# Optimization experiments

Hardware: AMD Instinct MI355X
Metric: run time of the kernel (lower is better)

Reference implementation:

```python
import jax, jax.numpy as jnp
import numpy as np

EPS = 1e-5

def _ln(x):
    # LayerNorm over last dim, no affine (elementwise_affine=False), biased variance
    mu = jnp.mean(x, axis=-1, keepdims=True)
    var = jnp.mean(jnp.square(x - mu), axis=-1, keepdims=True)
    return (x - mu) / jnp.sqrt(var + EPS)

def setup_inputs() -> dict:
    key = jax.random.key(0)
    B, I, H = 32768, 512, 512
    ks = jax.random.split(key, 12)
    std = 1.0 / np.sqrt(H)
    u = lambda k, shape: jax.random.uniform(k, shape, jnp.float32, -std, std)
    return {
        "x": jax.random.normal(ks[0], (B, I), jnp.float32),
        "h": jax.random.normal(ks[1], (B, H), jnp.float32),
        "W_i2h": u(ks[2], (I, 2 * H)),
        "b_i2h": u(ks[3], (2 * H,)),
        "W_h2h": u(ks[4], (H, 2 * H)),
        "b_h2h": u(ks[5], (2 * H,)),
        "W_hatW": u(ks[6], (I, H)),
        "b_hatW": u(ks[7], (H,)),
        "W_hatU": u(ks[8], (H, H)),
        "b_hatU": u(ks[9], (H,)),
    }

def reference(x, h, W_i2h, b_i2h, W_h2h, b_h2h, W_hatW, b_hatW, W_hatU, b_hatU):
    H = W_hatU.shape[0]
    i2h = _ln(x @ W_i2h + b_i2h)          # [B, 2H]
    h2h = _ln(h @ W_h2h + b_h2h)          # [B, 2H]
    gates = jax.nn.sigmoid(i2h + h2h)
    z_t = gates[:, :H]
    r_t = gates[:, -H:]
    h_hat_first = _ln(x @ W_hatW + b_hatW)  # [B, H]
    h_hat_last = _ln(h @ W_hatU + b_hatU)   # [B, H]
    h_hat = jnp.tanh(h_hat_first + r_t * h_hat_last)
    h_t = (1.0 - z_t) * h + z_t * h_hat
    return h_t
```

## Files before the change

kernel.cpp:

```cpp
#include <hip/hip_runtime.h>
#include <stdint.h>

typedef unsigned short u16;
typedef __attribute__((ext_vector_type(8))) short short8;
typedef __attribute__((ext_vector_type(4))) short short4v;
typedef __attribute__((ext_vector_type(4))) float f4;
typedef __attribute__((ext_vector_type(4))) float f32x4;

static __device__ __forceinline__ u16 f2b(float f) {
  union { float f; uint32_t u; } c; c.f = f;
  return (u16)((c.u + 0x7FFFu + ((c.u >> 16) & 1u)) >> 16);
}
static __device__ __forceinline__ float b2f(u16 s) {
  union { uint32_t u; float f; } c; c.u = ((uint32_t)s) << 16; return c.f;
}

__global__ __launch_bounds__(256) void cvt_kernel(const float* __restrict__ x,
                                                  const float* __restrict__ h,
                                                  u16* __restrict__ Ab) {
  const size_t half = (size_t)32768 * 512;
  size_t tid = (size_t)blockIdx.x * blockDim.x + threadIdx.x;
  size_t nth = (size_t)gridDim.x * blockDim.x;
  size_t total8 = (half * 2) >> 3;
  for (size_t t = tid; t < total8; t += nth) {
    size_t e = t << 3;
    const float* src = (e < half) ? (x + e) : (h + (e - half));
    f4 v0 = *(const f4*)src;
    f4 v1 = *(const f4*)(src + 4);
    short8 o;
    o[0] = (short)f2b(v0[0]); o[1] = (short)f2b(v0[1]);
    o[2] = (short)f2b(v0[2]); o[3] = (short)f2b(v0[3]);
    o[4] = (short)f2b(v1[0]); o[5] = (short)f2b(v1[1]);
    o[6] = (short)f2b(v1[2]); o[7] = (short)f2b(v1[3]);
    *(short8*)(Ab + e) = o;
  }
}

__global__ __launch_bounds__(256) void transpose_cat(const float* __restrict__ srcA,
                                                     const float* __restrict__ srcB,
                                                     u16* __restrict__ dst,
                                                     int NA, int NB) {
  __shared__ float t[32][33];
  int n0 = blockIdx.x * 32, k0 = blockIdx.y * 32;
  int tx = threadIdx.x, ty = threadIdx.y;
  const float* src; int strideN, nb;
  if (n0 < NA) { src = srcA; strideN = NA; nb = n0; }
  else         { src = srcB; strideN = NB; nb = n0 - NA; }
#pragma unroll
  for (int i = 0; i < 4; ++i) {
    int k = k0 + ty + i * 8;
    t[tx][ty + i * 8] = src[(size_t)k * strideN + nb + tx];
  }
  __syncthreads();
#pragma unroll
  for (int i = 0; i < 4; ++i) {
    int n = ty + i * 8;
    dst[(size_t)(n0 + n) * 512 + k0 + tx] = f2b(t[n][tx]);
  }
}

#define AS1 __attribute__((address_space(1)))
#define AS3 __attribute__((address_space(3)))
#define SBAR0 __builtin_amdgcn_sched_barrier(0)

__global__ __launch_bounds__(512, 2) void gemm_kernel(
    const u16* __restrict__ Ab, const u16* __restrict__ WxT,
    const u16* __restrict__ WhT, u16* __restrict__ Cb,
    int rowStartX, int rowStartH, int tilesPerHalf) {
  __shared__ u16 lds[65536];

  int tid = threadIdx.x, lane = tid & 63, wv = tid >> 6;
  int wm = wv >> 2, wn = wv & 3;
  int l15 = lane & 15, l4 = lane >> 4;

  int nwg = gridDim.x, bid = blockIdx.x;
  int swz = (nwg & 7) ? bid : ((bid & 7) * (nwg >> 3) + (bid >> 3));
  int mb = swz / 6, nb = swz - mb * 6;
  size_t m0; const u16* Wt;
  if (mb < tilesPerHalf) { m0 = (size_t)rowStartX + (size_t)mb * 256; Wt = WxT; }
  else { m0 = (size_t)rowStartH + (size_t)(mb - tilesPerHalf) * 256; Wt = WhT; }
  int crow0 = mb * 256, n0 = nb * 256;

  int rr = wv * 8 + (lane >> 3);
  int g8 = ((lane & 7) ^ (lane >> 3)) * 8;
  const u16* pA[4]; const u16* pB[4];
#pragma unroll
  for (int i = 0; i < 4; ++i) {
    pA[i] = Ab + (m0 + i * 64 + rr) * 512 + g8;
    pB[i] = Wt + (size_t)(n0 + i * 64 + rr) * 512 + g8;
  }
  int dst = wv * 512;

#define STG(t) do { \
    int _bb = ((t) & 1) << 15; \
    int _ko = (t) << 6; \
    _Pragma("unroll") \
    for (int i = 0; i < 4; ++i) { \
      __builtin_amdgcn_global_load_lds((const AS1 void*)(pA[i] + _ko), \
          (AS3 void*)(lds + _bb + i * 4096 + dst), 16, 0, 0); \
      __builtin_amdgcn_global_load_lds((const AS1 void*)(pB[i] + _ko), \
          (AS3 void*)(lds + _bb + 16384 + i * 4096 + dst), 16, 0, 0); \
    } \
  } while (0)

  int sl0 = (l4 ^ (l15 & 7)) * 8;
  int sl1 = ((4 + l4) ^ (l15 & 7)) * 8;
  int aRow = (wm * 128 + l15) * 64;
  int bRow = 16384 + (wn * 64 + l15) * 64;

  f32x4 acc[8][4] = {};

  STG(0); STG(1);
  asm volatile("s_waitcnt vmcnt(8)" ::: "memory");
  SBAR0; __builtin_amdgcn_s_barrier(); SBAR0;

  for (int t = 0; t < 8; ++t) {
    const u16* buf = lds + ((t & 1) << 15);
    short8 afr[4], bfr[4];
    if (t >= 1 && t < 7) STG(t + 1);
#pragma unroll
    for (int nr = 0; nr < 4; ++nr) bfr[nr] = *(const short8*)(buf + bRow + nr * 1024 + sl0);
#pragma unroll
    for (int mr = 0; mr < 4; ++mr) afr[mr] = *(const short8*)(buf + aRow + mr * 1024 + sl0);
    SBAR0; __builtin_amdgcn_s_barrier(); SBAR0;
    __builtin_amdgcn_s_setprio(1);
#pragma unroll
    for (int mr = 0; mr < 4; ++mr)
#pragma unroll
      for (int nr = 0; nr < 4; ++nr)
        acc[mr][nr] = __builtin_amdgcn_mfma_f32_16x16x32_bf16(bfr[nr], afr[mr], acc[mr][nr], 0, 0, 0);
    __builtin_amdgcn_s_setprio(0);
#pragma unroll
    for (int mr = 0; mr < 4; ++mr) afr[mr] = *(const short8*)(buf + aRow + (mr + 4) * 1024 + sl0);
    SBAR0; __builtin_amdgcn_s_barrier(); SBAR0;
    __builtin_amdgcn_s_setprio(1);
#pragma unroll
    for (int mr = 0; mr < 4; ++mr)
#pragma unroll
      for (int nr = 0; nr < 4; ++nr)
        acc[mr + 4][nr] = __builtin_amdgcn_mfma_f32_16x16x32_bf16(bfr[nr], afr[mr], acc[mr + 4][nr], 0, 0, 0);
    __builtin_amdgcn_s_setprio(0);
#pragma unroll
    for (int nr = 0; nr < 4; ++nr) bfr[nr] = *(const short8*)(buf + bRow + nr * 1024 + sl1);
#pragma unroll
    for (int mr = 0; mr < 4; ++mr) afr[mr] = *(const short8*)(buf + aRow + mr * 1024 + sl1);
    SBAR0; __builtin_amdgcn_s_barrier(); SBAR0;
    __builtin_amdgcn_s_setprio(1);
#pragma unroll
    for (int mr = 0; mr < 4; ++mr)
#pragma unroll
      for (int nr = 0; nr < 4; ++nr)
        acc[mr][nr] = __builtin_amdgcn_mfma_f32_16x16x32_bf16(bfr[nr], afr[mr], acc[mr][nr], 0, 0, 0);
    __builtin_amdgcn_s_setprio(0);
#pragma unroll
    for (int mr = 0; mr < 4; ++mr) afr[mr] = *(const short8*)(buf + aRow + (mr + 4) * 1024 + sl1);
    SBAR0; __builtin_amdgcn_s_barrier(); SBAR0;
    __builtin_amdgcn_s_setprio(1);
#pragma unroll
    for (int mr = 0; mr < 4; ++mr)
#pragma unroll
      for (int nr = 0; nr < 4; ++nr)
        acc[mr + 4][nr] = __builtin_amdgcn_mfma_f32_16x16x32_bf16(bfr[nr], afr[mr], acc[mr + 4][nr], 0, 0, 0);
    __builtin_amdgcn_s_setprio(0);
    SBAR0;
    if (t < 7) {
      asm volatile("s_waitcnt vmcnt(0)" ::: "memory");
      __builtin_amdgcn_s_barrier();
    }
    SBAR0;
  }
#undef STG

#pragma unroll
  for (int mr = 0; mr < 8; ++mr) {
    int m = crow0 + wm * 128 + mr * 16 + l15;
#pragma unroll
    for (int nr = 0; nr < 4; ++nr) {
      int n = n0 + wn * 64 + nr * 16 + l4 * 4;
      short4v o;
      o[0] = (short)f2b(acc[mr][nr][0]);
      o[1] = (short)f2b(acc[mr][nr][1]);
      o[2] = (short)f2b(acc[mr][nr][2]);
      o[3] = (short)f2b(acc[mr][nr][3]);
      *(short4v*)(Cb + (size_t)m * 1536 + n) = o;
    }
  }
}

__global__ __launch_bounds__(256) void epi_kernel(
    const u16* __restrict__ Cb, const float* __restrict__ h,
    const float* __restrict__ b_i2h, const float* __restrict__ b_h2h,
    const float* __restrict__ b_hatW, const float* __restrict__ b_hatU,
    float* __restrict__ out, int mBase, int BC) {
  int wv = threadIdx.x >> 6;
  int lane = threadIdx.x & 63;
  int mLocal = blockIdx.x * 4 + wv;
  size_t mGlob = (size_t)mBase + mLocal;
  const u16* Ar = Cb + (size_t)mLocal * 1536;
  const u16* Br = Cb + ((size_t)BC + mLocal) * 1536;
  int j0 = lane * 8;

  float a[3][8], b[3][8];
#pragma unroll
  for (int c = 0; c < 3; ++c) {
    short8 va = *(const short8*)(Ar + c * 512 + j0);
    short8 vb = *(const short8*)(Br + c * 512 + j0);
    const float* biasA = (c == 0) ? (b_i2h + j0) : (c == 1) ? (b_i2h + 512 + j0) : (b_hatW + j0);
    const float* biasB = (c == 0) ? (b_h2h + j0) : (c == 1) ? (b_h2h + 512 + j0) : (b_hatU + j0);
    f4 ba0 = *(const f4*)biasA, ba1 = *(const f4*)(biasA + 4);
    f4 bb0 = *(const f4*)biasB, bb1 = *(const f4*)(biasB + 4);
#pragma unroll
    for (int j = 0; j < 4; ++j) {
      a[c][j]     = b2f((u16)va[j])     + ba0[j];
      a[c][j + 4] = b2f((u16)va[j + 4]) + ba1[j];
      b[c][j]     = b2f((u16)vb[j])     + bb0[j];
      b[c][j + 4] = b2f((u16)vb[j + 4]) + bb1[j];
    }
  }

  float s1a = 0, q1a = 0, s2a = 0, q2a = 0, s1b = 0, q1b = 0, s2b = 0, q2b = 0;
#pragma unroll
  for (int j = 0; j < 8; ++j) {
    s1a += a[0][j] + a[1][j]; q1a += a[0][j] * a[0][j] + a[1][j] * a[1][j];
    s2a += a[2][j];           q2a += a[2][j] * a[2][j];
    s1b += b[0][j] + b[1][j]; q1b += b[0][j] * b[0][j] + b[1][j] * b[1][j];
    s2b += b[2][j];           q2b += b[2][j] * b[2][j];
  }
#pragma unroll
  for (int off = 32; off > 0; off >>= 1) {
    s1a += __shfl_xor(s1a, off); q1a += __shfl_xor(q1a, off);
    s2a += __shfl_xor(s2a, off); q2a += __shfl_xor(q2a, off);
    s1b += __shfl_xor(s1b, off); q1b += __shfl_xor(q1b, off);
    s2b += __shfl_xor(s2b, off); q2b += __shfl_xor(q2b, off);
  }
  const float inv1 = 1.0f / 1024.0f, inv2 = 1.0f / 512.0f, eps = 1e-5f;
  float mu1a = s1a * inv1, mu2a = s2a * inv2, mu1b = s1b * inv1, mu2b = s2b * inv2;
  float rs1a = rsqrtf(q1a * inv1 - mu1a * mu1a + eps);
  float rs2a = rsqrtf(q2a * inv2 - mu2a * mu2a + eps);
  float rs1b = rsqrtf(q1b * inv1 - mu1b * mu1b + eps);
  float rs2b = rsqrtf(q2b * inv2 - mu2b * mu2b + eps);

  const float* hrow = h + mGlob * 512 + j0;
  f4 h0 = *(const f4*)hrow, h1 = *(const f4*)(hrow + 4);
  f4 o0, o1;
#pragma unroll
  for (int j = 0; j < 8; ++j) {
    float zs  = (a[0][j] - mu1a) * rs1a + (b[0][j] - mu1b) * rs1b;
    float rsg = (a[1][j] - mu1a) * rs1a + (b[1][j] - mu1b) * rs1b;
    float z = 1.0f / (1.0f + __expf(-zs));
    float r = 1.0f / (1.0f + __expf(-rsg));
    float hh = tanhf((a[2][j] - mu2a) * rs2a + r * ((b[2][j] - mu2b) * rs2b));
    float hv = (j < 4) ? h0[j] : h1[j - 4];
    float o = hv + z * (hh - hv);
    if (j < 4) o0[j] = o; else o1[j - 4] = o;
  }
  *(f4*)(out + mGlob * 512 + j0) = o0;
  *(f4*)(out + mGlob * 512 + j0 + 4) = o1;
}

extern "C" void kernel_launch(void* const* d_in, const int* in_sizes, int n_in,
                              void* d_out, int out_size, void* d_ws, size_t ws_size,
                              hipStream_t stream) {
  const float* x      = (const float*)d_in[0];
  const float* h      = (const float*)d_in[1];
  const float* W_i2h  = (const float*)d_in[2];
  const float* b_i2h  = (const float*)d_in[3];
  const float* W_h2h  = (const float*)d_in[4];
  const float* b_h2h  = (const float*)d_in[5];
  const float* W_hatW = (const float*)d_in[6];
  const float* b_hatW = (const float*)d_in[7];
  const float* W_hatU = (const float*)d_in[8];
  const float* b_hatU = (const float*)d_in[9];
  float* out = (float*)d_out;

  u16* WxT = (u16*)d_ws;
  u16* WhT = WxT + (size_t)1536 * 512;
  u16* Ab  = WhT + (size_t)1536 * 512;
  u16* Cb  = Ab + (size_t)65536 * 512;

  size_t fixedElems = (size_t)2 * 1536 * 512 + (size_t)65536 * 512;
  int chunks = 1;
  for (;;) {
    size_t need = (fixedElems + (size_t)2 * (32768 / chunks) * 1536) * sizeof(u16);
    if (need <= ws_size || chunks >= 128) break;
    chunks <<= 1;
  }
  int BC = 32768 / chunks;
  int tph = BC / 256;
  int nwg = 2 * tph * 6;

  cvt_kernel<<<2048, 256, 0, stream>>>(x, h, Ab);
  transpose_cat<<<dim3(48, 16), dim3(32, 8), 0, stream>>>(W_i2h, W_hatW, WxT, 1024, 512);
  transpose_cat<<<dim3(48, 16), dim3(32, 8), 0, stream>>>(W_h2h, W_hatU, WhT, 1024, 512);
  for (int cc = 0; cc < chunks; ++cc) {
    gemm_kernel<<<nwg, 512, 0, stream>>>(Ab, WxT, WhT, Cb,
                                         cc * BC, 32768 + cc * BC, tph);
    epi_kernel<<<BC / 4, 256, 0, stream>>>(Cb, h, b_i2h, b_h2h, b_hatW, b_hatU,
                                           out, cc * BC, BC);
  }
}
```

Before: 246.5 us.

## Make GEMM persistent with 256x128 tiles and triple-buffered LDS pipeline

```diff
diff --git a/kernel.cpp b/kernel.cpp
--- a/kernel.cpp
+++ b/kernel.cpp
@@ -63,65 +63,77 @@
 #define AS3 __attribute__((address_space(3)))
 #define SBAR0 __builtin_amdgcn_sched_barrier(0)
 
-__global__ __launch_bounds__(512, 2) void gemm_kernel(
+__global__ __launch_bounds__(512, 1) void gemm_kernel(
     const u16* __restrict__ Ab, const u16* __restrict__ WxT,
     const u16* __restrict__ WhT, u16* __restrict__ Cb,
-    int rowStartX, int rowStartH, int tilesPerHalf) {
-  __shared__ u16 lds[65536];
+    int rowStartX, int rowStartH, int tphm, int KOT) {
+  __shared__ u16 lds[3 * 24576];
 
   int tid = threadIdx.x, lane = tid & 63, wv = tid >> 6;
-  int wm = wv >> 2, wn = wv & 3;
+  int wm = wv >> 1, wn = wv & 1;
   int l15 = lane & 15, l4 = lane >> 4;
 
   int nwg = gridDim.x, bid = blockIdx.x;
   int swz = (nwg & 7) ? bid : ((bid & 7) * (nwg >> 3) + (bid >> 3));
-  int mb = swz / 6, nb = swz - mb * 6;
-  size_t m0; const u16* Wt;
-  if (mb < tilesPerHalf) { m0 = (size_t)rowStartX + (size_t)mb * 256; Wt = WxT; }
-  else { m0 = (size_t)rowStartH + (size_t)(mb - tilesPerHalf) * 256; Wt = WhT; }
-  int crow0 = mb * 256, n0 = nb * 256;
-
-  int rr = wv * 8 + (lane >> 3);
-  int g8 = ((lane & 7) ^ (lane >> 3)) * 8;
-  const u16* pA[4]; const u16* pB[4];
-#pragma unroll
-  for (int i = 0; i < 4; ++i) {
-    pA[i] = Ab + (m0 + i * 64 + rr) * 512 + g8;
-    pB[i] = Wt + (size_t)(n0 + i * 64 + rr) * 512 + g8;
-  }
-  int dst = wv * 512;
-
-#define STG(t) do { \
-    int _bb = ((t) & 1) << 15; \
-    int _ko = (t) << 6; \
-    _Pragma("unroll") \
-    for (int i = 0; i < 4; ++i) { \
-      __builtin_amdgcn_global_load_lds((const AS1 void*)(pA[i] + _ko), \
-          (AS3 void*)(lds + _bb + i * 4096 + dst), 16, 0, 0); \
-      __builtin_amdgcn_global_load_lds((const AS1 void*)(pB[i] + _ko), \
-          (AS3 void*)(lds + _bb + 16384 + i * 4096 + dst), 16, 0, 0); \
-    } \
+
+  int stRow = tid >> 3;
+  int g8 = ((tid & 7) ^ (stRow & 7)) * 8;
+  int dOff = tid * 8;
+
+  const u16 *pA0, *pA1, *pA2, *pA3, *pB0, *pB1;
+#define SETSTAGE(o) do { \
+    int _ot = swz * KOT + (o); \
+    int _mb = _ot / 12, _nb = _ot - _mb * 12; \
+    size_t _am0 = (_mb < tphm) ? (size_t)rowStartX + (size_t)_mb * 256 \
+                               : (size_t)rowStartH + (size_t)(_mb - tphm) * 256; \
+    const u16* _Wt = (_mb < tphm) ? WxT : WhT; \
+    pA0 = Ab + (_am0 +   0 + stRow) * 512 + g8; \
+    pA1 = Ab + (_am0 +  64 + stRow) * 512 + g8; \
+    pA2 = Ab + (_am0 + 128 + stRow) * 512 + g8; \
+    pA3 = Ab + (_am0 + 192 + stRow) * 512 + g8; \
+    pB0 = _Wt + ((size_t)_nb * 128 +  0 + stRow) * 512 + g8; \
+    pB1 = _Wt + ((size_t)_nb * 128 + 64 + stRow) * 512 + g8; \
+  } while (0)
+
+#define STG(kt, bufq) do { \
+    u16* _b = lds + (bufq) * 24576; \
+    int _ko = (kt) << 6; \
+    __builtin_amdgcn_global_load_lds((const AS1 void*)(pA0 + _ko), (AS3 void*)(_b +  0    + dOff), 16, 0, 0); \
+    __builtin_amdgcn_global_load_lds((const AS1 void*)(pA1 + _ko), (AS3 void*)(_b + 4096  + dOff), 16, 0, 0); \
+    __builtin_amdgcn_global_load_lds((const AS1 void*)(pA2 + _ko), (AS3 void*)(_b + 8192  + dOff), 16, 0, 0); \
+    __builtin_amdgcn_global_load_lds((const AS1 void*)(pA3 + _ko), (AS3 void*)(_b + 12288 + dOff), 16, 0, 0); \
+    __builtin_amdgcn_global_load_lds((const AS1 void*)(pB0 + _ko), (AS3 void*)(_b + 16384 + dOff), 16, 0, 0); \
+    __builtin_amdgcn_global_load_lds((const AS1 void*)(pB1 + _ko), (AS3 void*)(_b + 20480 + dOff), 16, 0, 0); \
   } while (0)
 
   int sl0 = (l4 ^ (l15 & 7)) * 8;
   int sl1 = ((4 + l4) ^ (l15 & 7)) * 8;
-  int aRow = (wm * 128 + l15) * 64;
-  int bRow = 16384 + (wn * 64 + l15) * 64;
-
-  f32x4 acc[8][4] = {};
-
-  STG(0); STG(1);
-  asm volatile("s_waitcnt vmcnt(8)" ::: "memory");
+  int aOff = (wm * 64 + l15) * 64;
+  int bOff = 16384 + (wn * 64 + l15) * 64;
+
+  f32x4 acc[4][4] = {};
+
+  SETSTAGE(0);
+  STG(0, 0); STG(1, 1);
+  asm volatile("s_waitcnt vmcnt(6)" ::: "memory");
   SBAR0; __builtin_amdgcn_s_barrier(); SBAR0;
 
-  for (int t = 0; t < 8; ++t) {
-    const u16* buf = lds + ((t & 1) << 15);
+  int T = KOT * 8;
+  int bufC = 0;
+  for (int j = 0; j < T; ++j) {
+    u16* buf = lds + bufC * 24576;
+    int j2 = j + 2;
+    if (j2 < T) {
+      int kt2 = j2 & 7;
+      if (kt2 == 0) SETSTAGE(j2 >> 3);
+      int bufS = bufC - 1; if (bufS < 0) bufS = 2;
+      STG(kt2, bufS);
+    }
     short8 afr[4], bfr[4];
-    if (t >= 1 && t < 7) STG(t + 1);
-#pragma unroll
-    for (int nr = 0; nr < 4; ++nr) bfr[nr] = *(const short8*)(buf + bRow + nr * 1024 + sl0);
-#pragma unroll
-    for (int mr = 0; mr < 4; ++mr) afr[mr] = *(const short8*)(buf + aRow + mr * 1024 + sl0);
+#pragma unroll
+    for (int nr = 0; nr < 4; ++nr) bfr[nr] = *(const short8*)(buf + bOff + nr * 1024 + sl0);
+#pragma unroll
+    for (int mr = 0; mr < 4; ++mr) afr[mr] = *(const short8*)(buf + aOff + mr * 1024 + sl0);
     SBAR0; __builtin_amdgcn_s_barrier(); SBAR0;
     __builtin_amdgcn_s_setprio(1);
 #pragma unroll
@@ -131,19 +143,9 @@
         acc[mr][nr] = __builtin_amdgcn_mfma_f32_16x16x32_bf16(bfr[nr], afr[mr], acc[mr][nr], 0, 0, 0);
     __builtin_amdgcn_s_setprio(0);
 #pragma unroll
-    for (int mr = 0; mr < 4; ++mr) afr[mr] = *(const short8*)(buf + aRow + (mr + 4) * 1024 + sl0);
-    SBAR0; __builtin_amdgcn_s_barrier(); SBAR0;
-    __builtin_amdgcn_s_setprio(1);
-#pragma unroll
-    for (int mr = 0; mr < 4; ++mr)
-#pragma unroll
-      for (int nr = 0; nr < 4; ++nr)
-        acc[mr + 4][nr] = __builtin_amdgcn_mfma_f32_16x16x32_bf16(bfr[nr], afr[mr], acc[mr + 4][nr], 0, 0, 0);
-    __builtin_amdgcn_s_setprio(0);
-#pragma unroll
-    for (int nr = 0; nr < 4; ++nr) bfr[nr] = *(const short8*)(buf + bRow + nr * 1024 + sl1);
-#pragma unroll
-    for (int mr = 0; mr < 4; ++mr) afr[mr] = *(const short8*)(buf + aRow + mr * 1024 + sl1);
+    for (int nr = 0; nr < 4; ++nr) bfr[nr] = *(const short8*)(buf + bOff + nr * 1024 + sl1);
+#pragma unroll
+    for (int mr = 0; mr < 4; ++mr) afr[mr] = *(const short8*)(buf + aOff + mr * 1024 + sl1);
     SBAR0; __builtin_amdgcn_s_barrier(); SBAR0;
     __builtin_amdgcn_s_setprio(1);
 #pragma unroll
@@ -152,39 +154,37 @@
       for (int nr = 0; nr < 4; ++nr)
         acc[mr][nr] = __builtin_amdgcn_mfma_f32_16x16x32_bf16(bfr[nr], afr[mr], acc[mr][nr], 0, 0, 0);
     __builtin_amdgcn_s_setprio(0);
-#pragma unroll
-    for (int mr = 0; mr < 4; ++mr) afr[mr] = *(const short8*)(buf + aRow + (mr + 4) * 1024 + sl1);
-    SBAR0; __builtin_amdgcn_s_barrier(); SBAR0;
-    __builtin_amdgcn_s_setprio(1);
-#pragma unroll
-    for (int mr = 0; mr < 4; ++mr)
-#pragma unroll
-      for (int nr = 0; nr < 4; ++nr)
-        acc[mr + 4][nr] = __builtin_amdgcn_mfma_f32_16x16x32_bf16(bfr[nr], afr[mr], acc[mr + 4][nr], 0, 0, 0);
-    __builtin_amdgcn_s_setprio(0);
-    SBAR0;
-    if (t < 7) {
-      asm volatile("s_waitcnt vmcnt(0)" ::: "memory");
-      __builtin_amdgcn_s_barrier();
+    if ((j & 7) == 7) {
+      int ot = swz * KOT + (j >> 3);
+      int mb = ot / 12, nb = ot - mb * 12;
+      int crow0 = mb * 256, n0 = nb * 128;
+#pragma unroll
+      for (int mr = 0; mr < 4; ++mr) {
+        int m = crow0 + wm * 64 + mr * 16 + l15;
+#pragma unroll
+        for (int nr = 0; nr < 4; ++nr) {
+          int n = n0 + wn * 64 + nr * 16 + l4 * 4;
+          short4v o;
+          o[0] = (short)f2b(acc[mr][nr][0]);
+          o[1] = (short)f2b(acc[mr][nr][1]);
+          o[2] = (short)f2b(acc[mr][nr][2]);
+          o[3] = (short)f2b(acc[mr][nr][3]);
+          *(short4v*)(Cb + (size_t)m * 1536 + n) = o;
+          acc[mr][nr] = (f32x4)(0.0f);
+        }
+      }
     }
-    SBAR0;
+    if (j < T - 1) {
+      if (j2 < T) {
+        if ((j & 7) == 7) { asm volatile("s_waitcnt vmcnt(22)" ::: "memory"); }
+        else             { asm volatile("s_waitcnt vmcnt(6)"  ::: "memory"); }
+      } else             { asm volatile("s_waitcnt vmcnt(0)"  ::: "memory"); }
+      SBAR0; __builtin_amdgcn_s_barrier(); SBAR0;
+    }
+    bufC++; if (bufC == 3) bufC = 0;
   }
 #undef STG
-
-#pragma unroll
-  for (int mr = 0; mr < 8; ++mr) {
-    int m = crow0 + wm * 128 + mr * 16 + l15;
-#pragma unroll
-    for (int nr = 0; nr < 4; ++nr) {
-      int n = n0 + wn * 64 + nr * 16 + l4 * 4;
-      short4v o;
-      o[0] = (short)f2b(acc[mr][nr][0]);
-      o[1] = (short)f2b(acc[mr][nr][1]);
-      o[2] = (short)f2b(acc[mr][nr][2]);
-      o[3] = (short)f2b(acc[mr][nr][3]);
-      *(short4v*)(Cb + (size_t)m * 1536 + n) = o;
-    }
-  }
+#undef SETSTAGE
 }
 
 __global__ __launch_bounds__(256) void epi_kernel(
@@ -286,15 +286,18 @@
     chunks <<= 1;
   }
   int BC = 32768 / chunks;
-  int tph = BC / 256;
-  int nwg = 2 * tph * 6;
+  int tphm = BC / 256;
+  int totOt = 2 * tphm * 12;
+  int nwg = 256;
+  while (totOt % nwg) nwg >>= 1;
+  int KOT = totOt / nwg;
 
   cvt_kernel<<<2048, 256, 0, stream>>>(x, h, Ab);
   transpose_cat<<<dim3(48, 16), dim3(32, 8), 0, stream>>>(W_i2h, W_hatW, WxT, 1024, 512);
   transpose_cat<<<dim3(48, 16), dim3(32, 8), 0, stream>>>(W_h2h, W_hatU, WhT, 1024, 512);
   for (int cc = 0; cc < chunks; ++cc) {
     gemm_kernel<<<nwg, 512, 0, stream>>>(Ab, WxT, WhT, Cb,
-                                         cc * BC, 32768 + cc * BC, tph);
+                                         cc * BC, 32768 + cc * BC, tphm, KOT);
     epi_kernel<<<BC / 4, 256, 0, stream>>>(Cb, h, b_i2h, b_h2h, b_hatW, b_hatU,
                                            out, cc * BC, BC);
   }
```

Measured after the change: 261.3 us. 1.06x slower.
